# Performance work log

Measured on AMD Instinct MI355X. Metric: run time of the kernel, lower is better.

The kernel has to match this reference:

```python
import jax, jax.numpy as jnp
import numpy as np

B, S, H = 64, 1024, 1024

def setup_inputs() -> dict:
    key = jax.random.key(0)
    k1, k2, k3, k4, k5 = jax.random.split(key, 5)
    scale = 1.0 / np.sqrt(H)
    return {
        "decoder_state": jax.random.normal(k1, (B, H), dtype=jnp.float32),
        "encoder_outputs": jax.random.normal(k2, (B, S, H), dtype=jnp.float32),
        "mask": jnp.ones((B, S), dtype=jnp.int32),
        "W_s": jax.random.uniform(k3, (H, H), minval=-scale, maxval=scale, dtype=jnp.float32),
        "W_h": jax.random.uniform(k4, (H, H), minval=-scale, maxval=scale, dtype=jnp.float32),
        "v": jax.random.uniform(k5, (H,), minval=-scale, maxval=scale, dtype=jnp.float32),
    }

def reference(decoder_state, encoder_outputs, mask, W_s, W_h, v):
    # Additive (Bahdanau) attention.
    # proj_s: [B, H] -- original applies W_s to the expanded state (same math, computed once)
    proj_s = decoder_state @ W_s.T
    # proj_h: [B, S, H]
    proj_h = jnp.einsum('bsh,kh->bsk', encoder_outputs, W_h)
    energy = jnp.tanh(proj_s[:, None, :] + proj_h)          # [B, S, H]
    scores = jnp.einsum('bsh,h->bs', energy, v)             # [B, S]
    scores = jnp.where(mask == 0, -jnp.inf, scores)
    weights = jax.nn.softmax(scores, axis=-1)               # [B, S]
    context = jnp.einsum('bs,bsh->bh', weights, encoder_outputs)  # [B, H]
    return context, weights
```

## Files before the change

kernel.cpp:

```cpp
#include <hip/hip_runtime.h>
#include <hip/hip_bf16.h>

#define B_ 64
#define S_ 1024
#define H_ 1024
#define M_ (B_*S_)

typedef __attribute__((ext_vector_type(8))) short short8;
typedef __attribute__((ext_vector_type(4))) float f32x4;

__device__ __forceinline__ unsigned short f2bf(float f) {
    union { float f; unsigned u; } c; c.f = f;
    unsigned u = c.u;
    unsigned r = (u + 0x7fffu + ((u >> 16) & 1u)) >> 16;
    return (unsigned short)r;
}

__device__ __forceinline__ float bf2f(unsigned short h) {
    union { unsigned u; float f; } c; c.u = ((unsigned)h) << 16;
    return c.f;
}

__device__ __forceinline__ float tanh_fast(float x) {
    float t = __expf(2.0f * x);
    return 1.0f - 2.0f * __builtin_amdgcn_rcpf(t + 1.0f);
}

__device__ __forceinline__ void gll16(const unsigned short* g, unsigned short* l) {
    auto* gp = (const __attribute__((address_space(1))) unsigned short*)(g);
    auto* lp = (__attribute__((address_space(3))) unsigned short*)(l);
    __builtin_amdgcn_global_load_lds(gp, lp, 16, 0, 0);
}

__global__ void cvt_bf16_kernel(const float* __restrict__ src,
                                unsigned short* __restrict__ dst, int n8) {
    int idx = blockIdx.x * blockDim.x + threadIdx.x;
    int stride = gridDim.x * blockDim.x;
    for (int i = idx; i < n8; i += stride) {
        const float4* s4 = (const float4*)src + (size_t)i * 2;
        float4 a = s4[0], b = s4[1];
        short8 o;
        o[0] = f2bf(a.x); o[1] = f2bf(a.y); o[2] = f2bf(a.z); o[3] = f2bf(a.w);
        o[4] = f2bf(b.x); o[5] = f2bf(b.y); o[6] = f2bf(b.z); o[7] = f2bf(b.w);
        *((short8*)dst + i) = o;
    }
}

__global__ void proj_s_part_kernel(const float* __restrict__ dec,
                                   const float* __restrict__ Ws,
                                   float* __restrict__ part) {
    __shared__ float wss[64][68];
    const int kt = blockIdx.x & 15, hs = blockIdx.x >> 4;
    const int k0 = kt * 64, h0 = hs * 64;
    const int t = threadIdx.x;

    {
        const int r = t >> 2, c = (t & 3) * 16;
        const float4* src = (const float4*)(Ws + (size_t)(k0 + r) * H_ + h0 + c);
        float4 v0 = src[0], v1 = src[1], v2 = src[2], v3 = src[3];
        *(float4*)&wss[r][c + 0]  = v0;
        *(float4*)&wss[r][c + 4]  = v1;
        *(float4*)&wss[r][c + 8]  = v2;
        *(float4*)&wss[r][c + 12] = v3;
    }
    const int b = t >> 2, kq = t & 3;
    float4 dreg[16];
    const float4* dsrc = (const float4*)(dec + (size_t)b * H_ + h0);
#pragma unroll
    for (int i = 0; i < 16; ++i) dreg[i] = dsrc[i];
    __syncthreads();

    float acc[16] = {};
#pragma unroll
    for (int h4 = 0; h4 < 16; ++h4) {
        float4 d = dreg[h4];
#pragma unroll
        for (int j = 0; j < 16; ++j) {
            float4 wv = *(const float4*)&wss[kq + 4 * j][h4 * 4];
            acc[j] = fmaf(d.x, wv.x, acc[j]);
            acc[j] = fmaf(d.y, wv.y, acc[j]);
            acc[j] = fmaf(d.z, wv.z, acc[j]);
            acc[j] = fmaf(d.w, wv.w, acc[j]);
        }
    }
#pragma unroll
    for (int j = 0; j < 16; ++j)
        part[(size_t)hs * M_ + b * H_ + k0 + kq + 4 * j] = acc[j];
}

__global__ void proj_red_kernel(const float* __restrict__ part,
                                float* __restrict__ proj_s) {
    int i = blockIdx.x * 256 + threadIdx.x;
    float s = 0.0f;
#pragma unroll
    for (int p = 0; p < 16; ++p) s += part[(size_t)p * M_ + i];
    proj_s[i] = s;
}

__global__ void __launch_bounds__(512)
fused_scores_8p_kernel(const unsigned short* __restrict__ encb,
                       const unsigned short* __restrict__ Whb,
                       const float* __restrict__ proj_s,
                       const float* __restrict__ v,
                       float* __restrict__ scores_part) {
    __shared__ __align__(16) unsigned short Lsh[49152];

    const int bx0 = blockIdx.x;
    const int bx = (bx0 & 7) * 128 + (bx0 >> 3);
    const int nt = bx & 3;
    const int mt = bx >> 2;
    const int t = threadIdx.x;
    const int wid = t >> 6, lane = t & 63;
    const int wr = wid >> 2, wc = wid & 3;
    const int lrow = lane & 15, lgrp = lane >> 4;

    f32x4 acc[8][4] = {};

    const int srow = t >> 2;
    const int scol = ((t & 3) ^ ((t >> 3) & 3)) * 8;
    const unsigned short* gA = encb + (size_t)(mt * 256 + srow) * H_ + scol;
    const unsigned short* gB = Whb  + (size_t)(nt * 256 + srow) * H_ + scol;

    #define STAGE(bufb, op, h, kt) \
        gll16(((op) ? gB : gA) + (size_t)(h) * (128 * H_) + (kt) * 32, \
              Lsh + (bufb) * 16384 + (op) * 8192 + (h) * 4096 + wid * 512)

    int aoff[8], boff[4];
#pragma unroll
    for (int m = 0; m < 8; ++m) {
        int row = wr * 128 + m * 16 + lrow;
        aoff[m] = row * 64 + ((lgrp ^ ((row >> 1) & 3)) * 16);
    }
#pragma unroll
    for (int n = 0; n < 4; ++n) {
        int row = wc * 64 + n * 16 + lrow;
        boff[n] = row * 64 + ((lgrp ^ ((row >> 1) & 3)) * 16);
    }

    STAGE(0, 0, 0, 0); STAGE(0, 0, 1, 0); STAGE(0, 1, 0, 0); STAGE(0, 1, 1, 0);
    STAGE(1, 0, 0, 1); STAGE(1, 0, 1, 1); STAGE(1, 1, 0, 1); STAGE(1, 1, 1, 1);
    asm volatile("s_waitcnt vmcnt(4)" ::: "memory");
    __builtin_amdgcn_sched_barrier(0);
    __builtin_amdgcn_s_barrier();

    int bc = 0, bn = 2;
    for (int s = 0; s < 32; ++s) {
        const char* LA = (const char*)Lsh + bc * 32768;
        const char* LB = LA + 16384;
        const bool st = (s < 30);

        short8 af[4], bfr[4];
#pragma unroll
        for (int m = 0; m < 4; ++m)
            af[m] = *(const short8*)(LA + aoff[m]);
#pragma unroll
        for (int n = 0; n < 4; ++n)
            bfr[n] = *(const short8*)(LB + boff[n]);
        if (st) { STAGE(bn, 0, 0, s + 2); STAGE(bn, 0, 1, s + 2); }
        __builtin_amdgcn_s_barrier();
        __builtin_amdgcn_s_setprio(1);
#pragma unroll
        for (int m = 0; m < 4; ++m)
#pragma unroll
            for (int n = 0; n < 4; ++n)
                acc[m][n] = __builtin_amdgcn_mfma_f32_16x16x32_bf16(af[m], bfr[n], acc[m][n], 0, 0, 0);
        __builtin_amdgcn_s_setprio(0);
        __builtin_amdgcn_s_barrier();

        short8 af2[4];
#pragma unroll
        for (int m = 0; m < 4; ++m)
            af2[m] = *(const short8*)(LA + aoff[4 + m]);
        if (st) { STAGE(bn, 1, 0, s + 2); STAGE(bn, 1, 1, s + 2); }
        __builtin_amdgcn_s_barrier();
        __builtin_amdgcn_s_setprio(1);
#pragma unroll
        for (int m = 0; m < 4; ++m)
#pragma unroll
            for (int n = 0; n < 4; ++n)
                acc[4 + m][n] = __builtin_amdgcn_mfma_f32_16x16x32_bf16(af2[m], bfr[n], acc[4 + m][n], 0, 0, 0);
        __builtin_amdgcn_s_setprio(0);
        __builtin_amdgcn_s_barrier();

        if (s <= 29) { asm volatile("s_waitcnt vmcnt(4)" ::: "memory"); }
        else         { asm volatile("s_waitcnt vmcnt(0)" ::: "memory"); }
        __builtin_amdgcn_sched_barrier(0);
        __builtin_amdgcn_s_barrier();
        bc = (bc == 2) ? 0 : bc + 1;
        bn = (bn == 2) ? 0 : bn + 1;
    }
    #undef STAGE

    const int b = mt >> 2;
    float vv[4], ps[4];
#pragma unroll
    for (int n = 0; n < 4; ++n) {
        int col = nt * 256 + wc * 64 + n * 16 + lrow;
        vv[n] = v[col];
        ps[n] = proj_s[b * H_ + col];
    }
    float* sums = (float*)Lsh;
#pragma unroll
    for (int m = 0; m < 8; ++m) {
#pragma unroll
        for (int j = 0; j < 4; ++j) {
            float s = 0.0f;
#pragma unroll
            for (int n = 0; n < 4; ++n)
                s = fmaf(tanh_fast(acc[m][n][j] + ps[n]), vv[n], s);
            s += __shfl_xor(s, 1, 64);
            s += __shfl_xor(s, 2, 64);
            s += __shfl_xor(s, 4, 64);
            s += __shfl_xor(s, 8, 64);
            if (lrow == 0)
                sums[(wr * 128 + m * 16 + lgrp * 4 + j) * 4 + wc] = s;
        }
    }
    __syncthreads();
    if (t < 256) {
        float r = sums[t * 4 + 0] + sums[t * 4 + 1] + sums[t * 4 + 2] + sums[t * 4 + 3];
        scores_part[(size_t)nt * M_ + mt * 256 + t] = r;
    }
}

__global__ void fused_scores_kernel(const float* __restrict__ enc,
                                    const float* __restrict__ Wh,
                                    const float* __restrict__ proj_s,
                                    const float* __restrict__ v,
                                    float* __restrict__ scores_part) {
    __shared__ __align__(16) unsigned short As[128][40];
    __shared__ __align__(16) unsigned short Bs[128][40];
    __shared__ float sums[128][2];

    const int bx = blockIdx.x;
    const int nt = bx & 7;
    const int mt = bx >> 3;
    const int t = threadIdx.x;
    const int w = t >> 6, lane = t & 63;
    const int wr = w >> 1, wc = w & 1;
    const int lrow = lane & 15, lgrp = lane >> 4;

    f32x4 acc[4][4] = {};

    const int srow = t >> 1;
    const int shalf = t & 1;
    const float* gA = enc + (size_t)(mt * 128 + srow) * H_ + shalf * 16;
    const float* gB = Wh  + (size_t)(nt * 128 + srow) * H_ + shalf * 16;
    unsigned short* lA = &As[srow][shalf * 16];
    unsigned short* lB = &Bs[srow][shalf * 16];

    for (int kt = 0; kt < H_ / 32; ++kt) {
        __syncthreads();
        const float4* a4 = (const float4*)(gA + kt * 32);
        const float4* b4 = (const float4*)(gB + kt * 32);
        union { unsigned short us[16]; uint4 q[2]; } pa, pb;
#pragma unroll
        for (int i = 0; i < 4; ++i) {
            float4 av = a4[i];
            float4 bv = b4[i];
            pa.us[i*4+0] = f2bf(av.x); pa.us[i*4+1] = f2bf(av.y);
            pa.us[i*4+2] = f2bf(av.z); pa.us[i*4+3] = f2bf(av.w);
            pb.us[i*4+0] = f2bf(bv.x); pb.us[i*4+1] = f2bf(bv.y);
            pb.us[i*4+2] = f2bf(bv.z); pb.us[i*4+3] = f2bf(bv.w);
        }
        *(uint4*)(lA)     = pa.q[0];
        *(uint4*)(lA + 8) = pa.q[1];
        *(uint4*)(lB)     = pb.q[0];
        *(uint4*)(lB + 8) = pb.q[1];
        __syncthreads();

        short8 af[4], bf[4];
#pragma unroll
        for (int m = 0; m < 4; ++m)
            af[m] = *(const short8*)&As[wr * 64 + m * 16 + lrow][lgrp * 8];
#pragma unroll
        for (int n = 0; n < 4; ++n)
            bf[n] = *(const short8*)&Bs[wc * 64 + n * 16 + lrow][lgrp * 8];
#pragma unroll
        for (int m = 0; m < 4; ++m)
#pragma unroll
            for (int n = 0; n < 4; ++n)
                acc[m][n] = __builtin_amdgcn_mfma_f32_16x16x32_bf16(af[m], bf[n], acc[m][n], 0, 0, 0);
    }

    const int b = mt >> 3;
    float vv[4], ps[4];
#pragma unroll
    for (int n = 0; n < 4; ++n) {
        int col = nt * 128 + wc * 64 + n * 16 + lrow;
        vv[n] = v[col];
        ps[n] = proj_s[b * H_ + col];
    }
    float rs[4][4];
#pragma unroll
    for (int m = 0; m < 4; ++m) {
#pragma unroll
        for (int j = 0; j < 4; ++j) {
            float s = 0.0f;
#pragma unroll
            for (int n = 0; n < 4; ++n)
                s = fmaf(tanh_fast(acc[m][n][j] + ps[n]), vv[n], s);
            s += __shfl_xor(s, 1, 64);
            s += __shfl_xor(s, 2, 64);
            s += __shfl_xor(s, 4, 64);
            s += __shfl_xor(s, 8, 64);
            rs[m][j] = s;
        }
    }
    if (lrow == 0) {
#pragma unroll
        for (int m = 0; m < 4; ++m)
#pragma unroll
            for (int j = 0; j < 4; ++j)
                sums[wr * 64 + m * 16 + lgrp * 4 + j][wc] = rs[m][j];
    }
    __syncthreads();
    if (t < 128)
        scores_part[(size_t)nt * M_ + mt * 128 + t] = sums[t][0] + sums[t][1];
}

__global__ void softmax_kernel(const float* __restrict__ scores_part,
                               const int* __restrict__ mask,
                               float* __restrict__ weights, int np) {
    const int b = blockIdx.x, t = threadIdx.x;
    __shared__ float red[8];
    float sc[4];
#pragma unroll
    for (int i = 0; i < 4; ++i) {
        int s = t + i * 256;
        float x = 0.0f;
        for (int p = 0; p < np; ++p)
            x += scores_part[(size_t)p * M_ + b * S_ + s];
        if (mask[b * S_ + s] == 0) x = -INFINITY;
        sc[i] = x;
    }
    float mx = fmaxf(fmaxf(sc[0], sc[1]), fmaxf(sc[2], sc[3]));
#pragma unroll
    for (int m = 32; m >= 1; m >>= 1) mx = fmaxf(mx, __shfl_xor(mx, m, 64));
    if ((t & 63) == 0) red[t >> 6] = mx;
    __syncthreads();
    mx = fmaxf(fmaxf(red[0], red[1]), fmaxf(red[2], red[3]));

    float e[4]; float sum = 0.0f;
#pragma unroll
    for (int i = 0; i < 4; ++i) { e[i] = __expf(sc[i] - mx); sum += e[i]; }
#pragma unroll
    for (int m = 32; m >= 1; m >>= 1) sum += __shfl_xor(sum, m, 64);
    if ((t & 63) == 0) red[4 + (t >> 6)] = sum;
    __syncthreads();
    sum = red[4] + red[5] + red[6] + red[7];
    float inv = 1.0f / sum;
#pragma unroll
    for (int i = 0; i < 4; ++i)
        weights[b * S_ + t + i * 256] = e[i] * inv;
}

__global__ void context_part_bf16_kernel(const unsigned short* __restrict__ encb,
                                         const float* __restrict__ weights,
                                         float* __restrict__ ctx_part) {
    const int b = blockIdx.x >> 5;
    const int sc = blockIdx.x & 31;
    const int t = threadIdx.x;
    __shared__ float wv[32];
    if (t < 32) wv[t] = weights[b * S_ + sc * 32 + t];
    __syncthreads();
    const short8* e8 = (const short8*)(encb + (size_t)(b * S_ + sc * 32) * H_) + t;
    float a[8] = {};
#pragma unroll 4
    for (int i = 0; i < 32; ++i) {
        short8 ev = e8[(size_t)i * 128];
        float w = wv[i];
#pragma unroll
        for (int j = 0; j < 8; ++j)
            a[j] = fmaf(w, bf2f((unsigned short)ev[j]), a[j]);
    }
    float* dst = ctx_part + (size_t)sc * M_ + b * H_ + t * 8;
    float4 o0; o0.x = a[0]; o0.y = a[1]; o0.z = a[2]; o0.w = a[3];
    float4 o1; o1.x = a[4]; o1.y = a[5]; o1.z = a[6]; o1.w = a[7];
    *(float4*)dst = o0;
    *(float4*)(dst + 4) = o1;
}

__global__ void context_part_kernel(const float* __restrict__ enc,
                                    const float* __restrict__ weights,
                                    float* __restrict__ ctx_part) {
    const int b = blockIdx.x >> 4;
    const int sc = blockIdx.x & 15;
    const int t = threadIdx.x;
    __shared__ float wv[64];
    if (t < 64) wv[t] = weights[b * S_ + sc * 64 + t];
    __syncthreads();
    const float4* e4 = (const float4*)(enc + (size_t)(b * S_ + sc * 64) * H_) + t;
    float ax = 0.f, ay = 0.f, az = 0.f, aw = 0.f;
#pragma unroll 4
    for (int i = 0; i < 64; ++i) {
        float4 ev = e4[i * 256];
        float wgt = wv[i];
        ax = fmaf(wgt, ev.x, ax);
        ay = fmaf(wgt, ev.y, ay);
        az = fmaf(wgt, ev.z, az);
        aw = fmaf(wgt, ev.w, aw);
    }
    float4 o; o.x = ax; o.y = ay; o.z = az; o.w = aw;
    *((float4*)(ctx_part + (size_t)sc * M_ + b * H_) + t) = o;
}

__global__ void ctx_reduce_kernel(const float* __restrict__ ctx_part,
                                  float* __restrict__ ctx, int np) {
    int idx = blockIdx.x * 256 + threadIdx.x;
    float s = 0.0f;
    for (int p = 0; p < np; ++p) s += ctx_part[(size_t)p * M_ + idx];
    ctx[idx] = s;
}

extern "C" void kernel_launch(void* const* d_in, const int* in_sizes, int n_in,
                              void* d_out, int out_size, void* d_ws, size_t ws_size,
                              hipStream_t stream) {
    const float* dec  = (const float*)d_in[0];
    const float* enc  = (const float*)d_in[1];
    const int*   mask = (const int*)d_in[2];
    const float* Ws   = (const float*)d_in[3];
    const float* Wh   = (const float*)d_in[4];
    const float* v    = (const float*)d_in[5];

    float* out = (float*)d_out;

    float* proj_s      = (float*)d_ws;
    float* proj_part   = proj_s + M_;
    float* scores_part = proj_part + 16 * (size_t)M_;
    float* ctx_part    = scores_part + 8 * (size_t)M_;
    unsigned short* encb = (unsigned short*)(ctx_part + 32 * (size_t)M_);
    unsigned short* Whb  = encb + (size_t)B_ * S_ * H_;

    const size_t need_small = 4ull * (1 + 16 + 8 + 32) * M_;
    const size_t need_big   = need_small + 2ull * ((size_t)B_ * S_ * H_ + (size_t)H_ * H_);

    proj_s_part_kernel<<<256, 256, 0, stream>>>(dec, Ws, proj_part);
    proj_red_kernel<<<256, 256, 0, stream>>>(proj_part, proj_s);

    if (ws_size >= need_big) {
        cvt_bf16_kernel<<<2048, 256, 0, stream>>>(enc, encb, B_ * S_ * H_ / 8);
        cvt_bf16_kernel<<<512, 256, 0, stream>>>(Wh, Whb, H_ * H_ / 8);
        fused_scores_8p_kernel<<<1024, 512, 0, stream>>>(encb, Whb, proj_s, v, scores_part);
        softmax_kernel<<<64, 256, 0, stream>>>(scores_part, mask, out + M_, 4);
        context_part_bf16_kernel<<<2048, 128, 0, stream>>>(encb, out + M_, ctx_part);
        ctx_reduce_kernel<<<256, 256, 0, stream>>>(ctx_part, out, 32);
    } else {
        fused_scores_kernel<<<4096, 256, 0, stream>>>(enc, Wh, proj_s, v, scores_part);
        softmax_kernel<<<64, 256, 0, stream>>>(scores_part, mask, out + M_, 8);
        context_part_kernel<<<1024, 256, 0, stream>>>(enc, out + M_, ctx_part);
        ctx_reduce_kernel<<<256, 256, 0, stream>>>(ctx_part, out, 16);
    }
}
```

Before: 270.1 us.

## Use K=64 double-buffered LDS tiles with 8-way swizzle in fused scores GEMM

Result: faster. 261.0 us (-3.3%).

```diff
diff --git a/kernel.cpp b/kernel.cpp
--- a/kernel.cpp
+++ b/kernel.cpp
@@ -98,12 +98,12 @@
 }
 
 __global__ void __launch_bounds__(512)
-fused_scores_8p_kernel(const unsigned short* __restrict__ encb,
-                       const unsigned short* __restrict__ Whb,
-                       const float* __restrict__ proj_s,
-                       const float* __restrict__ v,
-                       float* __restrict__ scores_part) {
-    __shared__ __align__(16) unsigned short Lsh[49152];
+fused_scores_k64_kernel(const unsigned short* __restrict__ encb,
+                        const unsigned short* __restrict__ Whb,
+                        const float* __restrict__ proj_s,
+                        const float* __restrict__ v,
+                        float* __restrict__ scores_part) {
+    __shared__ __align__(16) unsigned short Lsh[65536];
 
     const int bx0 = blockIdx.x;
     const int bx = (bx0 & 7) * 128 + (bx0 >> 3);
@@ -116,80 +116,103 @@
 
     f32x4 acc[8][4] = {};
 
-    const int srow = t >> 2;
-    const int scol = ((t & 3) ^ ((t >> 3) & 3)) * 8;
-    const unsigned short* gA = encb + (size_t)(mt * 256 + srow) * H_ + scol;
-    const unsigned short* gB = Whb  + (size_t)(nt * 256 + srow) * H_ + scol;
-
-    #define STAGE(bufb, op, h, kt) \
-        gll16(((op) ? gB : gA) + (size_t)(h) * (128 * H_) + (kt) * 32, \
-              Lsh + (bufb) * 16384 + (op) * 8192 + (h) * 4096 + wid * 512)
+    const int srow = t >> 3;
+    const int sgran = (t & 7) ^ (srow & 7);
+    const unsigned short* gA = encb + (size_t)(mt * 256 + srow) * H_ + sgran * 8;
+    const unsigned short* gB = Whb  + (size_t)(nt * 256 + srow) * H_ + sgran * 8;
+
+#define STG(bb, op, g, kt) \
+    gll16(((op) ? gB : gA) + (size_t)(g) * 64 * H_ + (kt) * 64, \
+          Lsh + (bb) * 32768 + (op) * 16384 + (g) * 4096 + wid * 512)
 
     int aoff[8], boff[4];
 #pragma unroll
     for (int m = 0; m < 8; ++m) {
         int row = wr * 128 + m * 16 + lrow;
-        aoff[m] = row * 64 + ((lgrp ^ ((row >> 1) & 3)) * 16);
+        aoff[m] = row * 64 + (lgrp ^ (row & 7)) * 8;
     }
 #pragma unroll
     for (int n = 0; n < 4; ++n) {
         int row = wc * 64 + n * 16 + lrow;
-        boff[n] = row * 64 + ((lgrp ^ ((row >> 1) & 3)) * 16);
-    }
-
-    STAGE(0, 0, 0, 0); STAGE(0, 0, 1, 0); STAGE(0, 1, 0, 0); STAGE(0, 1, 1, 0);
-    STAGE(1, 0, 0, 1); STAGE(1, 0, 1, 1); STAGE(1, 1, 0, 1); STAGE(1, 1, 1, 1);
-    asm volatile("s_waitcnt vmcnt(4)" ::: "memory");
+        boff[n] = 16384 + row * 64 + (lgrp ^ (row & 7)) * 8;
+    }
+
+    STG(0,1,0,0); STG(0,1,1,0); STG(0,1,2,0); STG(0,1,3,0);
+    STG(0,0,0,0); STG(0,0,1,0); STG(0,0,2,0); STG(0,0,3,0);
+    asm volatile("s_waitcnt vmcnt(0)" ::: "memory");
     __builtin_amdgcn_sched_barrier(0);
     __builtin_amdgcn_s_barrier();
 
-    int bc = 0, bn = 2;
-    for (int s = 0; s < 32; ++s) {
-        const char* LA = (const char*)Lsh + bc * 32768;
-        const char* LB = LA + 16384;
-        const bool st = (s < 30);
-
-        short8 af[4], bfr[4];
-#pragma unroll
-        for (int m = 0; m < 4; ++m)
-            af[m] = *(const short8*)(LA + aoff[m]);
-#pragma unroll
-        for (int n = 0; n < 4; ++n)
-            bfr[n] = *(const short8*)(LB + boff[n]);
-        if (st) { STAGE(bn, 0, 0, s + 2); STAGE(bn, 0, 1, s + 2); }
+    int buf = 0;
+    for (int s = 0; s < 16; ++s) {
+        const int hb = buf * 32768;
+        const int sb = buf ^ 1;
+        const bool st = (s < 15);
+        short8 a0[4], a1[4], b0[4], b1[4];
+
+#pragma unroll
+        for (int m = 0; m < 4; ++m) a0[m] = *(const short8*)&Lsh[hb + aoff[m]];
+#pragma unroll
+        for (int n = 0; n < 4; ++n) b0[n] = *(const short8*)&Lsh[hb + boff[n]];
+        if (st) { STG(sb,1,0,s+1); STG(sb,1,1,s+1); STG(sb,1,2,s+1); STG(sb,1,3,s+1);
+                  STG(sb,0,0,s+1); STG(sb,0,2,s+1); }
         __builtin_amdgcn_s_barrier();
         __builtin_amdgcn_s_setprio(1);
 #pragma unroll
         for (int m = 0; m < 4; ++m)
 #pragma unroll
             for (int n = 0; n < 4; ++n)
-                acc[m][n] = __builtin_amdgcn_mfma_f32_16x16x32_bf16(af[m], bfr[n], acc[m][n], 0, 0, 0);
+                acc[m][n] = __builtin_amdgcn_mfma_f32_16x16x32_bf16(a0[m], b0[n], acc[m][n], 0, 0, 0);
         __builtin_amdgcn_s_setprio(0);
-        __builtin_amdgcn_s_barrier();
-
-        short8 af2[4];
-#pragma unroll
-        for (int m = 0; m < 4; ++m)
-            af2[m] = *(const short8*)(LA + aoff[4 + m]);
-        if (st) { STAGE(bn, 1, 0, s + 2); STAGE(bn, 1, 1, s + 2); }
+        if (st) { asm volatile("s_waitcnt vmcnt(6)" ::: "memory"); }
+        else    { asm volatile("s_waitcnt vmcnt(0)" ::: "memory"); }
+        __builtin_amdgcn_sched_barrier(0);
+        __builtin_amdgcn_s_barrier();
+
+#pragma unroll
+        for (int m = 0; m < 4; ++m) a1[m] = *(const short8*)&Lsh[hb + aoff[4 + m]];
+        if (st) { STG(sb,0,1,s+1); STG(sb,0,3,s+1); }
         __builtin_amdgcn_s_barrier();
         __builtin_amdgcn_s_setprio(1);
 #pragma unroll
         for (int m = 0; m < 4; ++m)
 #pragma unroll
             for (int n = 0; n < 4; ++n)
-                acc[4 + m][n] = __builtin_amdgcn_mfma_f32_16x16x32_bf16(af2[m], bfr[n], acc[4 + m][n], 0, 0, 0);
+                acc[4 + m][n] = __builtin_amdgcn_mfma_f32_16x16x32_bf16(a1[m], b0[n], acc[4 + m][n], 0, 0, 0);
         __builtin_amdgcn_s_setprio(0);
         __builtin_amdgcn_s_barrier();
 
-        if (s <= 29) { asm volatile("s_waitcnt vmcnt(4)" ::: "memory"); }
-        else         { asm volatile("s_waitcnt vmcnt(0)" ::: "memory"); }
+#pragma unroll
+        for (int m = 0; m < 4; ++m) a0[m] = *(const short8*)&Lsh[hb + (aoff[m] ^ 32)];
+#pragma unroll
+        for (int n = 0; n < 4; ++n) b1[n] = *(const short8*)&Lsh[hb + (boff[n] ^ 32)];
+        __builtin_amdgcn_s_barrier();
+        __builtin_amdgcn_s_setprio(1);
+#pragma unroll
+        for (int m = 0; m < 4; ++m)
+#pragma unroll
+            for (int n = 0; n < 4; ++n)
+                acc[m][n] = __builtin_amdgcn_mfma_f32_16x16x32_bf16(a0[m], b1[n], acc[m][n], 0, 0, 0);
+        __builtin_amdgcn_s_setprio(0);
+        __builtin_amdgcn_s_barrier();
+
+#pragma unroll
+        for (int m = 0; m < 4; ++m) a1[m] = *(const short8*)&Lsh[hb + (aoff[4 + m] ^ 32)];
+        __builtin_amdgcn_s_barrier();
+        __builtin_amdgcn_s_setprio(1);
+#pragma unroll
+        for (int m = 0; m < 4; ++m)
+#pragma unroll
+            for (int n = 0; n < 4; ++n)
+                acc[4 + m][n] = __builtin_amdgcn_mfma_f32_16x16x32_bf16(a1[m], b1[n], acc[4 + m][n], 0, 0, 0);
+        __builtin_amdgcn_s_setprio(0);
+        if (st) { asm volatile("s_waitcnt vmcnt(2)" ::: "memory"); }
+        else    { asm volatile("s_waitcnt vmcnt(0)" ::: "memory"); }
         __builtin_amdgcn_sched_barrier(0);
         __builtin_amdgcn_s_barrier();
-        bc = (bc == 2) ? 0 : bc + 1;
-        bn = (bn == 2) ? 0 : bn + 1;
-    }
-    #undef STAGE
+        buf ^= 1;
+    }
+#undef STG
 
     const int b = mt >> 2;
     float vv[4], ps[4];
@@ -441,7 +464,7 @@
     if (ws_size >= need_big) {
         cvt_bf16_kernel<<<2048, 256, 0, stream>>>(enc, encb, B_ * S_ * H_ / 8);
         cvt_bf16_kernel<<<512, 256, 0, stream>>>(Wh, Whb, H_ * H_ / 8);
-        fused_scores_8p_kernel<<<1024, 512, 0, stream>>>(encb, Whb, proj_s, v, scores_part);
+        fused_scores_k64_kernel<<<1024, 512, 0, stream>>>(encb, Whb, proj_s, v, scores_part);
         softmax_kernel<<<64, 256, 0, stream>>>(scores_part, mask, out + M_, 4);
         context_part_bf16_kernel<<<2048, 128, 0, stream>>>(encb, out + M_, ctx_part);
         ctx_reduce_kernel<<<256, 256, 0, stream>>>(ctx_part, out, 32);
```
